# Optimization experiments

Measured on AMD Instinct MI355X. Metric: run time of the kernel, lower is better.

The kernel has to match this reference:

```python
import jax, jax.numpy as jnp
import numpy as np

N_USERS = 4096
N_ITEMS = 4096
D = 64  # embedding_dim / out_features
N = N_USERS + N_ITEMS
ALPHA = 0.2  # LeakyReLU slope
NEG_INF = jnp.float32(-9e15)


def setup_inputs() -> dict:
    key = jax.random.key(0)
    ks = jax.random.split(key, 11)
    s = 0.05  # xavier-ish scale
    rn = lambda k, shape: jax.random.normal(k, shape, jnp.float32) * s
    adj = jax.random.randint(ks[0], (N, N), 0, 2, jnp.int32)
    return {
        "adj": adj,
        "user_emb": rn(ks[1], (N_USERS, D)),
        "item_emb": rn(ks[2], (N_ITEMS, D)),
        "W0_w": rn(ks[3], (D, D)), "W0_b": rn(ks[4], (D,)), "a0": rn(ks[5], (2 * D, 1)),
        "W1_w": rn(ks[6], (D, D)), "W1_b": rn(ks[7], (D,)), "a1": rn(ks[8], (2 * D, 1)),
        "out_w": rn(ks[9], (D, D)), "out_b": rn(ks[10], (D,)),
    }


def gat_layer(x, adj, W_w, W_b, a):
    # Wh: [N, D]
    Wh = x @ W_w.T + W_b
    # Original materializes [N,N,2D] concat then matmul with a.
    # Algebraically identical: e_ij = leakyrelu(a1 . Wh_i + a2 . Wh_j)
    src = Wh @ a[:D]          # [N, 1] -> row contribution
    dst = (Wh @ a[D:]).T      # [1, N] -> column contribution
    e = jax.nn.leaky_relu(src + dst, ALPHA)        # [N, N]
    e = jnp.where(adj > 0, e, NEG_INF)
    att = jax.nn.softmax(e, axis=1)                # dropout=0.0 (eval)
    return att @ Wh                                 # [N, D]


def reference(adj, user_emb, item_emb, W0_w, W0_b, a0, W1_w, W1_b, a1, out_w, out_b):
    x = jnp.concatenate([user_emb, item_emb], axis=0)  # [N, D]
    x = jax.nn.relu(gat_layer(x, adj, W0_w, W0_b, a0))
    x = jax.nn.relu(gat_layer(x, adj, W1_w, W1_b, a1))
    u, it = x[:N_USERS], x[N_USERS:]
    return (u @ out_w.T + out_b, it @ out_w.T + out_b)
```

## Files before the change

kernel.cpp:

```cpp
#include <hip/hip_runtime.h>


typedef _Float16 f16x8 __attribute__((ext_vector_type(8)));
typedef _Float16 f16x2 __attribute__((ext_vector_type(2)));
typedef float    f32x16 __attribute__((ext_vector_type(16)));

union Frag16 {
    f16x8        v;
    unsigned int u[4];
};
union HV2 {
    f16x2        v;
    _Float16     h[2];
    unsigned int u;
};

__global__ __launch_bounds__(256) void k_pack(
    const int* __restrict__ adj, unsigned long long* __restrict__ bits)
{
    int wgid = blockIdx.x * 4 + (threadIdx.x >> 6);
    int lane = threadIdx.x & 63;
    const long long NW  = 2048LL * 4;
    const long long TOT = 8192LL * 8192;
    for (long long base = (long long)wgid * 512; base < TOT; base += NW * 512) {
        int a[8];
#pragma unroll
        for (int i = 0; i < 8; i++) a[i] = adj[base + i * 64 + lane];
        unsigned long long m[8];
#pragma unroll
        for (int i = 0; i < 8; i++) m[i] = __ballot(a[i] != 0);
        if (lane < 4) {
            reinterpret_cast<ulonglong2*>(bits + (base >> 6))[lane] =
                ulonglong2{m[2 * lane], m[2 * lane + 1]};
        }
    }
}

__device__ __forceinline__ void prep_tail(
    float (*xs)[65], float (*Wt)[65], float (*sred)[64], float (*dred)[64],
    const float* __restrict__ W, const float* __restrict__ bias,
    const float* __restrict__ avec,
    _Float16* __restrict__ WhT,
    unsigned int* __restrict__ E12,
    _Float16* __restrict__ F1h, _Float16* __restrict__ F2h,
    int tid, int r0)
{
    for (int e = tid; e < 4096; e += 256) {
        int o = e >> 6, c = e & 63;
        Wt[c][o] = W[e];
    }
    __syncthreads();

    int r = tid & 63, chunk = tid >> 6, c0 = chunk * 16;
    float acc[16];
#pragma unroll
    for (int o = 0; o < 16; o++) acc[o] = bias[c0 + o];
    for (int c = 0; c < 64; c++) {
        float xv = xs[r][c];
#pragma unroll
        for (int o = 0; o < 16; o++) acc[o] += xv * Wt[c][c0 + o];
    }

    float sp = 0.f, dp = 0.f;
#pragma unroll
    for (int o = 0; o < 16; o++) {
        sp += acc[o] * avec[c0 + o];
        dp += acc[o] * avec[64 + c0 + o];
    }
    sred[chunk][r] = sp;
    dred[chunk][r] = dp;

#pragma unroll
    for (int o = 0; o < 16; o++)
        WhT[(size_t)(c0 + o) * 8192 + r0 + r] = (_Float16)acc[o];

    __syncthreads();
    if (tid < 64) {
        int g = r0 + tid;
        float s = sred[0][tid] + sred[1][tid] + sred[2][tid] + sred[3][tid];
        float d = dred[0][tid] + dred[1][tid] + dred[2][tid] + dred[3][tid];
        HV2 e;
        e.h[0] = (_Float16)__expf(s);
        e.h[1] = (_Float16)__expf(0.2f * s);
        E12[g] = e.u;
        F1h[g] = (_Float16)__expf(d);
        F2h[g] = (_Float16)__expf(0.2f * d);
    }
}

__global__ __launch_bounds__(256) void k_prep0(
    const float* __restrict__ ue, const float* __restrict__ ie,
    const float* __restrict__ W, const float* __restrict__ bias,
    const float* __restrict__ avec,
    _Float16* __restrict__ WhT, unsigned int* __restrict__ E12,
    _Float16* __restrict__ F1h, _Float16* __restrict__ F2h)
{
    __shared__ float xs[64][65];
    __shared__ float Wt[64][65];
    __shared__ float sred[4][64];
    __shared__ float dred[4][64];
    int tid = threadIdx.x, r0 = blockIdx.x * 64;

    for (int e = tid; e < 4096; e += 256) {
        int r = e >> 6, c = e & 63;
        int row = r0 + r;
        xs[r][c] = (row < 4096) ? ue[row * 64 + c] : ie[(row - 4096) * 64 + c];
    }
    prep_tail(xs, Wt, sred, dred, W, bias, avec, WhT, E12, F1h, F2h, tid, r0);
}

template <int NS>
__global__ __launch_bounds__(256) void k_prep1(
    const float* __restrict__ numP, const float* __restrict__ denP,
    const float* __restrict__ W, const float* __restrict__ bias,
    const float* __restrict__ avec,
    _Float16* __restrict__ WhT, unsigned int* __restrict__ E12,
    _Float16* __restrict__ F1h, _Float16* __restrict__ F2h)
{
    __shared__ float xs[64][65];
    __shared__ float Wt[64][65];
    __shared__ float sred[4][64];
    __shared__ float dred[4][64];
    __shared__ float dtot[64];
    int tid = threadIdx.x, r0 = blockIdx.x * 64;
    int rb128 = blockIdx.x >> 1, half = blockIdx.x & 1;

    if (tid < 64) {
        float s = 0.f;
#pragma unroll
        for (int p = 0; p < NS; p++) s += denP[p * 8192 + r0 + tid];
        dtot[tid] = fmaxf(s, 1e-20f);
    }
    __syncthreads();
    for (int e = tid; e < 4096; e += 256) {
        int r = e >> 6;
        float s = 0.f;
#pragma unroll
        for (int p = 0; p < NS; p++)
            s += numP[(size_t)(p * 64 + rb128) * 8192 + half * 4096 + e];
        float v = s / dtot[r];
        xs[r][e & 63] = v > 0.f ? v : 0.f;
    }
    prep_tail(xs, Wt, sred, dred, W, bias, avec, WhT, E12, F1h, F2h, tid, r0);
}

struct AggSmem {
    uint4        WhBf[1024];
    unsigned int mkAll[128][20];
    unsigned int f1All[256];
    unsigned int f2All[256];
};

__device__ __forceinline__ void agg_body(
    const unsigned int* __restrict__ bits,
    const _Float16* __restrict__ WhT, const unsigned int* __restrict__ E12,
    const _Float16* __restrict__ F1h, const _Float16* __restrict__ F2h,
    float* __restrict__ numP, float* __restrict__ denP)
{
    constexpr int CK = 128, NCH = 4;
    __shared__ AggSmem sm;

    int tid  = threadIdx.x;
    int wave = tid >> 6, lane = tid & 63;
    int l32 = lane & 31, khalf = lane >> 5;
    int rowblk = blockIdx.x, ks = blockIdx.y;
    int k0 = ks * (CK * NCH);

#pragma unroll
    for (int j = 0; j < 2; j++) {
        int s = tid + 256 * j;
        int row_l = s >> 2, q = s & 3;
        uint4 v = *reinterpret_cast<const uint4*>(
            bits + (size_t)(rowblk * 128 + row_l) * 256 + ks * 16 + q * 4);
        *reinterpret_cast<uint4*>(&sm.mkAll[row_l][q * 4]) = v;
    }
    if (tid < 64) {
        uint4 v = *reinterpret_cast<const uint4*>(F1h + k0 + tid * 8);
        *reinterpret_cast<uint4*>(&sm.f1All[tid * 4]) = v;
    } else if (tid < 128) {
        int t2 = tid - 64;
        uint4 v = *reinterpret_cast<const uint4*>(F2h + k0 + t2 * 8);
        *reinterpret_cast<uint4*>(&sm.f2All[t2 * 4]) = v;
    }

    uint4 P[4];
#pragma unroll
    for (int i = 0; i < 4; i++) {
        int ff = (tid >> 3) + (i & 1) * 32, gg = (tid & 7) + (i >> 1) * 8;
        P[i] = *reinterpret_cast<const uint4*>(WhT + (size_t)ff * 8192 + k0 + gg * 8);
    }
#pragma unroll
    for (int i = 0; i < 4; i++) {
        int ff = (tid >> 3) + (i & 1) * 32, gg = (tid & 7) + (i >> 1) * 8;
        sm.WhBf[gg * 64 + ((ff + gg) & 63)] = P[i];
    }
    __syncthreads();

    int row = rowblk * 128 + wave * 32 + l32;
    int lrow = wave * 32 + l32;
    unsigned int e12 = E12[row];
    HV2 e1p, e2p;
    e1p.u = (e12 & 0xFFFFu);  e1p.u |= e1p.u << 16;
    e2p.u = (e12 >> 16);      e2p.u |= e2p.u << 16;

    f32x16 acc0 = {}, acc1 = {}, accd = {};

    Frag16 ones;
    ones.u[0] = ones.u[1] = ones.u[2] = ones.u[3] = 0x3C003C00u;

    for (int c = 0; c < NCH; c++) {
        if (c + 1 < NCH) {
            int kc = k0 + (c + 1) * CK;
#pragma unroll
            for (int i = 0; i < 4; i++) {
                int ff = (tid >> 3) + (i & 1) * 32, gg = (tid & 7) + (i >> 1) * 8;
                P[i] = *reinterpret_cast<const uint4*>(
                    WhT + (size_t)ff * 8192 + kc + gg * 8);
            }
        }

#pragma unroll
        for (int kb = 0; kb < CK; kb += 16) {
            int wi = kb + khalf * 8;
            unsigned int word = sm.mkAll[lrow][c * 4 + (wi >> 5)];
            unsigned int w8 = word >> (wi & 31);

            int fidx = (c * CK + wi) >> 1;
            uint4 f1v = *reinterpret_cast<const uint4*>(&sm.f1All[fidx]);
            uint4 f2v = *reinterpret_cast<const uint4*>(&sm.f2All[fidx]);
            unsigned int f1a[4] = {f1v.x, f1v.y, f1v.z, f1v.w};
            unsigned int f2a[4] = {f2v.x, f2v.y, f2v.z, f2v.w};

            Frag16 A;
#pragma unroll
            for (int p = 0; p < 4; p++) {
                HV2 fa, fb, wa;
                fa.u = f1a[p];
                fb.u = f2a[p];
                wa.v = __builtin_elementwise_max(e1p.v * fa.v, e2p.v * fb.v);
                int s0 = ((int)(w8 << (31 - 2 * p))) >> 31;
                int s1 = ((int)(w8 << (30 - 2 * p))) >> 31;
                unsigned int pm = ((unsigned)s0 & 0xFFFFu) | ((unsigned)s1 << 16);
                A.u[p] = wa.u & pm;
            }

            int g0 = (kb >> 3) + khalf;
            Frag16 B0, B1;
            B0.v = *reinterpret_cast<const f16x8*>(
                &sm.WhBf[g0 * 64 + ((l32 + g0) & 63)]);
            B1.v = *reinterpret_cast<const f16x8*>(
                &sm.WhBf[g0 * 64 + ((32 + l32 + g0) & 63)]);
            acc0 = __builtin_amdgcn_mfma_f32_32x32x16_f16(A.v, B0.v, acc0, 0, 0, 0);
            acc1 = __builtin_amdgcn_mfma_f32_32x32x16_f16(A.v, B1.v, acc1, 0, 0, 0);
            accd = __builtin_amdgcn_mfma_f32_32x32x16_f16(A.v, ones.v, accd, 0, 0, 0);
        }

        if (c + 1 < NCH) {
            __syncthreads();
#pragma unroll
            for (int i = 0; i < 4; i++) {
                int ff = (tid >> 3) + (i & 1) * 32, gg = (tid & 7) + (i >> 1) * 8;
                sm.WhBf[gg * 64 + ((ff + gg) & 63)] = P[i];
            }
            __syncthreads();
        }
    }

    float* tile = numP + (size_t)(ks * 64 + rowblk) * 8192;
#pragma unroll
    for (int r = 0; r < 16; r++) {
        int rl = wave * 32 + (r & 3) + 8 * (r >> 2) + 4 * khalf;
        tile[rl * 64 + l32]      = acc0[r];
        tile[rl * 64 + 32 + l32] = acc1[r];
        if (l32 == 0)
            denP[ks * 8192 + rowblk * 128 + rl] = accd[r];
    }
}

__global__ __launch_bounds__(256) void k_agg_l0(
    const unsigned int* __restrict__ bits,
    const _Float16* __restrict__ WhT, const unsigned int* __restrict__ E12,
    const _Float16* __restrict__ F1h, const _Float16* __restrict__ F2h,
    float* __restrict__ numP, float* __restrict__ denP)
{
    agg_body(bits, WhT, E12, F1h, F2h, numP, denP);
}

__global__ __launch_bounds__(256) void k_agg_l1(
    const unsigned int* __restrict__ bits,
    const _Float16* __restrict__ WhT, const unsigned int* __restrict__ E12,
    const _Float16* __restrict__ F1h, const _Float16* __restrict__ F2h,
    float* __restrict__ numP, float* __restrict__ denP)
{
    agg_body(bits, WhT, E12, F1h, F2h, numP, denP);
}

template <int NS>
__global__ __launch_bounds__(256) void k_out(
    const float* __restrict__ numP, const float* __restrict__ denP,
    const float* __restrict__ W, const float* __restrict__ bias,
    float* __restrict__ out)
{
    __shared__ float xs[64][65];
    __shared__ float Wt[64][65];
    __shared__ float dtot[64];
    int tid = threadIdx.x, r0 = blockIdx.x * 64;
    int rb128 = blockIdx.x >> 1, half = blockIdx.x & 1;

    if (tid < 64) {
        float s = 0.f;
#pragma unroll
        for (int p = 0; p < NS; p++) s += denP[p * 8192 + r0 + tid];
        dtot[tid] = fmaxf(s, 1e-20f);
    }
    __syncthreads();
    for (int e = tid; e < 4096; e += 256) {
        int r = e >> 6;
        float s = 0.f;
#pragma unroll
        for (int p = 0; p < NS; p++)
            s += numP[(size_t)(p * 64 + rb128) * 8192 + half * 4096 + e];
        float v = s / dtot[r];
        xs[r][e & 63] = v > 0.f ? v : 0.f;
    }
    for (int e = tid; e < 4096; e += 256) {
        int o = e >> 6, c = e & 63;
        Wt[c][o] = W[e];
    }
    __syncthreads();

    int r = tid & 63, chunk = tid >> 6, c0 = chunk * 16;
    float acc[16];
#pragma unroll
    for (int o = 0; o < 16; o++) acc[o] = bias[c0 + o];
    for (int c = 0; c < 64; c++) {
        float xv = xs[r][c];
#pragma unroll
        for (int o = 0; o < 16; o++) acc[o] += xv * Wt[c][c0 + o];
    }
#pragma unroll
    for (int o = 0; o < 16; o++)
        out[(r0 + r) * 64 + c0 + o] = acc[o];
}

extern "C" void kernel_launch(void* const* d_in, const int* in_sizes, int n_in,
                              void* d_out, int out_size, void* d_ws, size_t ws_size,
                              hipStream_t stream)
{
    const int*   adj = (const int*)d_in[0];
    const float* ue  = (const float*)d_in[1];
    const float* ie  = (const float*)d_in[2];
    const float* W0w = (const float*)d_in[3];
    const float* W0b = (const float*)d_in[4];
    const float* a0  = (const float*)d_in[5];
    const float* W1w = (const float*)d_in[6];
    const float* W1b = (const float*)d_in[7];
    const float* a1  = (const float*)d_in[8];
    const float* Ow  = (const float*)d_in[9];
    const float* Ob  = (const float*)d_in[10];

    constexpr int NS = 16;

    char* ws = (char*)d_ws;
    size_t off = 0;
    auto alloc = [&](size_t bytes) -> char* {
        char* p = ws + off;
        off += (bytes + 255) & ~(size_t)255;
        return p;
    };
    float*        numP    = (float*)alloc((size_t)NS * 64 * 8192 * 4);
    float*        denP    = (float*)alloc((size_t)NS * 8192 * 4);
    unsigned long long* adjbits = (unsigned long long*)alloc(8192 * 1024);
    _Float16*     WhT0    = (_Float16*)alloc(64 * 8192 * 2);
    _Float16*     WhT1    = (_Float16*)alloc(64 * 8192 * 2);
    unsigned int* E12_0   = (unsigned int*)alloc(8192 * 4);
    unsigned int* E12_1   = (unsigned int*)alloc(8192 * 4);
    _Float16* F1h0 = (_Float16*)alloc(8192 * 2);
    _Float16* F2h0 = (_Float16*)alloc(8192 * 2);
    _Float16* F1h1 = (_Float16*)alloc(8192 * 2);
    _Float16* F2h1 = (_Float16*)alloc(8192 * 2);

    const unsigned int* bits32 = (const unsigned int*)adjbits;

    k_pack<<<2048, 256, 0, stream>>>(adj, adjbits);

    k_prep0<<<128, 256, 0, stream>>>(ue, ie, W0w, W0b, a0,
                                     WhT0, E12_0, F1h0, F2h0);
    k_agg_l0<<<dim3(64, NS), 256, 0, stream>>>(bits32, WhT0, E12_0,
                                               F1h0, F2h0, numP, denP);
    k_prep1<NS><<<128, 256, 0, stream>>>(numP, denP, W1w, W1b, a1,
                                         WhT1, E12_1, F1h1, F2h1);
    k_agg_l1<<<dim3(64, NS), 256, 0, stream>>>(bits32, WhT1, E12_1,
                                               F1h1, F2h1, numP, denP);
    k_out<NS><<<128, 256, 0, stream>>>(numP, denP, Ow, Ob, (float*)d_out);
}
```

Before: 477.9 us.

## Fuse adjacency bit-packing into first aggregation kernel

Removes the standalone k_pack launch and has the layer-0 aggregation kernel read the int32 adjacency tile for its own rows and column chunk. It ballots the tile into bitmasks directly into shared memory and also writes them out for layer 1. This saves a kernel launch and a separate full pass over the adjacency that re-read the bits. The cost is a serial 16-step load/ballot loop at the start of each agg block, which may expose memory latency that the standalone pack kernel hid with more parallelism.

```diff
diff --git a/kernel.cpp b/kernel.cpp
--- a/kernel.cpp
+++ b/kernel.cpp
@@ -14,27 +14,6 @@
     _Float16     h[2];
     unsigned int u;
 };
-
-__global__ __launch_bounds__(256) void k_pack(
-    const int* __restrict__ adj, unsigned long long* __restrict__ bits)
-{
-    int wgid = blockIdx.x * 4 + (threadIdx.x >> 6);
-    int lane = threadIdx.x & 63;
-    const long long NW  = 2048LL * 4;
-    const long long TOT = 8192LL * 8192;
-    for (long long base = (long long)wgid * 512; base < TOT; base += NW * 512) {
-        int a[8];
-#pragma unroll
-        for (int i = 0; i < 8; i++) a[i] = adj[base + i * 64 + lane];
-        unsigned long long m[8];
-#pragma unroll
-        for (int i = 0; i < 8; i++) m[i] = __ballot(a[i] != 0);
-        if (lane < 4) {
-            reinterpret_cast<ulonglong2*>(bits + (base >> 6))[lane] =
-                ulonglong2{m[2 * lane], m[2 * lane + 1]};
-        }
-    }
-}
 
 __device__ __forceinline__ void prep_tail(
     float (*xs)[65], float (*Wt)[65], float (*sred)[64], float (*dred)[64],
@@ -151,7 +130,10 @@
     unsigned int f2All[256];
 };
 
+template <bool BUILD>
 __device__ __forceinline__ void agg_body(
+    const int* __restrict__ adj,
+    unsigned long long* __restrict__ bitsOut,
     const unsigned int* __restrict__ bits,
     const _Float16* __restrict__ WhT, const unsigned int* __restrict__ E12,
     const _Float16* __restrict__ F1h, const _Float16* __restrict__ F2h,
@@ -166,14 +148,13 @@
     int rowblk = blockIdx.x, ks = blockIdx.y;
     int k0 = ks * (CK * NCH);
 
-#pragma unroll
-    for (int j = 0; j < 2; j++) {
-        int s = tid + 256 * j;
-        int row_l = s >> 2, q = s & 3;
-        uint4 v = *reinterpret_cast<const uint4*>(
-            bits + (size_t)(rowblk * 128 + row_l) * 256 + ks * 16 + q * 4);
-        *reinterpret_cast<uint4*>(&sm.mkAll[row_l][q * 4]) = v;
-    }
+    uint4 P[4];
+#pragma unroll
+    for (int i = 0; i < 4; i++) {
+        int ff = (tid >> 3) + (i & 1) * 32, gg = (tid & 7) + (i >> 1) * 8;
+        P[i] = *reinterpret_cast<const uint4*>(WhT + (size_t)ff * 8192 + k0 + gg * 8);
+    }
+
     if (tid < 64) {
         uint4 v = *reinterpret_cast<const uint4*>(F1h + k0 + tid * 8);
         *reinterpret_cast<uint4*>(&sm.f1All[tid * 4]) = v;
@@ -183,12 +164,44 @@
         *reinterpret_cast<uint4*>(&sm.f2All[t2 * 4]) = v;
     }
 
-    uint4 P[4];
-#pragma unroll
-    for (int i = 0; i < 4; i++) {
-        int ff = (tid >> 3) + (i & 1) * 32, gg = (tid & 7) + (i >> 1) * 8;
-        P[i] = *reinterpret_cast<const uint4*>(WhT + (size_t)ff * 8192 + k0 + gg * 8);
-    }
+    if constexpr (BUILD) {
+        int rbase = rowblk * 128;
+        for (int t = 0; t < 32; t += 2) {
+            int ra = wave * 32 + t;
+            const int* apa = adj + (size_t)(rbase + ra) * 8192 + k0;
+            const int* apb = apa + 8192;
+            int a0[8], a1[8];
+#pragma unroll
+            for (int j = 0; j < 8; j++) a0[j] = apa[j * 64 + lane];
+#pragma unroll
+            for (int j = 0; j < 8; j++) a1[j] = apb[j * 64 + lane];
+            unsigned long long m0[8], m1[8];
+#pragma unroll
+            for (int j = 0; j < 8; j++) m0[j] = __ballot(a0[j] != 0);
+#pragma unroll
+            for (int j = 0; j < 8; j++) m1[j] = __ballot(a1[j] != 0);
+            if (lane < 4) {
+                ulonglong2 v0{m0[2 * lane], m0[2 * lane + 1]};
+                ulonglong2 v1{m1[2 * lane], m1[2 * lane + 1]};
+                *reinterpret_cast<ulonglong2*>(&sm.mkAll[ra][lane * 4])     = v0;
+                *reinterpret_cast<ulonglong2*>(&sm.mkAll[ra + 1][lane * 4]) = v1;
+                reinterpret_cast<ulonglong2*>(
+                    bitsOut + (((size_t)(rbase + ra)) << 7) + ks * 8)[lane] = v0;
+                reinterpret_cast<ulonglong2*>(
+                    bitsOut + (((size_t)(rbase + ra + 1)) << 7) + ks * 8)[lane] = v1;
+            }
+        }
+    } else {
+#pragma unroll
+        for (int j = 0; j < 2; j++) {
+            int s = tid + 256 * j;
+            int row_l = s >> 2, q = s & 3;
+            uint4 v = *reinterpret_cast<const uint4*>(
+                bits + (size_t)(rowblk * 128 + row_l) * 256 + ks * 16 + q * 4);
+            *reinterpret_cast<uint4*>(&sm.mkAll[row_l][q * 4]) = v;
+        }
+    }
+
 #pragma unroll
     for (int i = 0; i < 4; i++) {
         int ff = (tid >> 3) + (i & 1) * 32, gg = (tid & 7) + (i >> 1) * 8;
@@ -278,12 +291,12 @@
 }
 
 __global__ __launch_bounds__(256) void k_agg_l0(
-    const unsigned int* __restrict__ bits,
+    const int* __restrict__ adj, unsigned long long* __restrict__ bitsOut,
     const _Float16* __restrict__ WhT, const unsigned int* __restrict__ E12,
     const _Float16* __restrict__ F1h, const _Float16* __restrict__ F2h,
     float* __restrict__ numP, float* __restrict__ denP)
 {
-    agg_body(bits, WhT, E12, F1h, F2h, numP, denP);
+    agg_body<true>(adj, bitsOut, nullptr, WhT, E12, F1h, F2h, numP, denP);
 }
 
 __global__ __launch_bounds__(256) void k_agg_l1(
@@ -292,7 +305,7 @@
     const _Float16* __restrict__ F1h, const _Float16* __restrict__ F2h,
     float* __restrict__ numP, float* __restrict__ denP)
 {
-    agg_body(bits, WhT, E12, F1h, F2h, numP, denP);
+    agg_body<false>(nullptr, nullptr, bits, WhT, E12, F1h, F2h, numP, denP);
 }
 
 template <int NS>
@@ -382,11 +395,9 @@
 
     const unsigned int* bits32 = (const unsigned int*)adjbits;
 
-    k_pack<<<2048, 256, 0, stream>>>(adj, adjbits);
-
     k_prep0<<<128, 256, 0, stream>>>(ue, ie, W0w, W0b, a0,
                                      WhT0, E12_0, F1h0, F2h0);
-    k_agg_l0<<<dim3(64, NS), 256, 0, stream>>>(bits32, WhT0, E12_0,
+    k_agg_l0<<<dim3(64, NS), 256, 0, stream>>>(adj, adjbits, WhT0, E12_0,
                                                F1h0, F2h0, numP, denP);
     k_prep1<NS><<<128, 256, 0, stream>>>(numP, denP, W1w, W1b, a1,
                                          WhT1, E12_1, F1h1, F2h1);
```

After: 474.5 us. No clear change (-0.7%).
